# Kernel optimization log

Measured on AMD Instinct MI355X. Metric: run time of the kernel, lower is better.

## Reference

```python
import jax, jax.numpy as jnp
import numpy as np

B, T, F, H = 128, 1024, 256, 512  # batch, seq_len (input_dims[0]), features (input_dims[1]), rnn_size


def _lstm(xWb, U, reverse=False, return_sequences=False):
    """Keras-semantics LSTM. xWb: [B,T,4H] = x @ W + b precomputed. Gate order i,f,g,o."""
    Hn = U.shape[0]
    xs = jnp.swapaxes(xWb, 0, 1)  # [T,B,4H] for scan over time
    h0 = jnp.zeros((xWb.shape[0], Hn), xWb.dtype)
    c0 = h0

    def step(carry, xw):
        h, c = carry
        z = xw + h @ U  # [B,4H]
        i, f, g, o = jnp.split(z, 4, axis=-1)
        i = jax.nn.sigmoid(i)
        f = jax.nn.sigmoid(f)
        g = jnp.tanh(g)
        o = jax.nn.sigmoid(o)
        c = f * c + i * g
        h = o * jnp.tanh(c)
        return (h, c), h

    (hT, _), hs = jax.lax.scan(step, (h0, c0), xs, reverse=reverse)
    if return_sequences:
        return jnp.swapaxes(hs, 0, 1)  # [B,T,H]
    return hT  # [B,H] final state (for reverse=True this is the state after t=0)


def setup_inputs() -> dict:
    key = jax.random.key(0)
    ks = jax.random.split(key, 9)
    g = lambda k, shape: (jax.random.normal(k, shape, jnp.float32) * 0.05)
    return {
        "x": jax.random.uniform(ks[0], (B, T, F), jnp.float32),
        # encoder forward-direction LSTM
        "Wf": g(ks[1], (F, 4 * H)), "Uf": g(ks[2], (H, 4 * H)), "bf": jnp.zeros((4 * H,), jnp.float32),
        # encoder backward-direction LSTM
        "Wb": g(ks[3], (F, 4 * H)), "Ub": g(ks[4], (H, 4 * H)), "bb": jnp.zeros((4 * H,), jnp.float32),
        # decoder LSTM (input is concat latent, 2H wide)
        "Wd": g(ks[5], (2 * H, 4 * H)), "Ud": g(ks[6], (H, 4 * H)), "bd": jnp.zeros((4 * H,), jnp.float32),
        # TimeDistributed Dense
        "Wo": g(ks[7], (H, F)), "bo": jnp.zeros((F,), jnp.float32),
    }


def reference(x, Wf, Uf, bf, Wb, Ub, bb, Wd, Ud, bd, Wo, bo):
    # Encoder: Bidirectional(LSTM(H)) -> concat final states [B, 2H]
    h_fwd = _lstm(x @ Wf + bf, Uf, reverse=False)
    h_bwd = _lstm(x @ Wb + bb, Ub, reverse=True)
    latent = jnp.concatenate([h_fwd, h_bwd], axis=-1)  # [B, 2H]
    # Decoder: RepeatVector(T) -> LSTM(H, return_sequences) -> TimeDistributed(Dense(F))
    rep = jnp.broadcast_to(latent[:, None, :], (x.shape[0], x.shape[1], 2 * H))  # [B,T,2H]
    dec = _lstm(rep @ Wd + bd, Ud, return_sequences=True)  # [B,T,H]
    return dec @ Wo + bo  # [B,T,F]
```

## Files before the change

### kernel.cpp

```cpp
#include <hip/hip_runtime.h>
#include <stdint.h>

typedef unsigned short u16;
typedef short bf16x8 __attribute__((ext_vector_type(8)));
typedef float f32x4  __attribute__((ext_vector_type(4)));
typedef unsigned short u16x8 __attribute__((ext_vector_type(8)));
typedef unsigned int   u32x4 __attribute__((ext_vector_type(4)));

__device__ __forceinline__ u16 f2bf(float f) {
  uint32_t u = __float_as_uint(f);
  return (u16)((u + 0x7FFFu + ((u >> 16) & 1u)) >> 16);
}
__device__ __forceinline__ float fsig(float x) {
  x = fminf(fmaxf(x, -30.f), 30.f);
  return __builtin_amdgcn_rcpf(1.f + __builtin_amdgcn_exp2f(-1.44269504088896f * x));
}
__device__ __forceinline__ float ftanhf(float x) {
  x = fminf(fmaxf(x, -10.f), 10.f);
  float e = __builtin_amdgcn_exp2f(2.88539008177793f * x);
  return (e - 1.f) * __builtin_amdgcn_rcpf(e + 1.f);
}

__device__ __forceinline__ int flag_load(const int* p) {
  int v;
  asm volatile("global_load_dword %0, %1, off sc0 sc1\n\ts_waitcnt vmcnt(0)"
               : "=v"(v) : "v"(p) : "memory");
  return v;
}
__device__ __forceinline__ void flag_store(int* p, int v) {
  asm volatile("global_store_dword %0, %1, off sc0 sc1" :: "v"(p), "v"(v) : "memory");
}
__device__ __forceinline__ uint4 ld_coh_x4(const u16* p) {
  uint4 v;
  asm volatile("global_load_dwordx4 %0, %1, off sc0 sc1" : "=v"(v) : "v"(p) : "memory");
  return v;
}
__device__ __forceinline__ void st_coh_x4(u16* p, u32x4 v) {
  asm volatile("global_store_dwordx4 %0, %1, off sc0 sc1" :: "v"(p), "v"(v) : "memory");
}
__device__ __forceinline__ uint4 ld_x4(const float* p) {
  uint4 v;
  asm volatile("global_load_dwordx4 %0, %1, off" : "=v"(v) : "v"(p) : "memory");
  return v;
}
__device__ __forceinline__ void wait_vm0() {
  asm volatile("s_waitcnt vmcnt(0)" ::: "memory");
}
__device__ __forceinline__ bf16x8 pin_frag(const u16* p) {
  uint4 v;
  asm volatile("global_load_dwordx4 %0, %1, off" : "=v"(v) : "v"(p));
  return __builtin_bit_cast(bf16x8, v);
}
__device__ __forceinline__ void poll_flag(const int* fp, int target) {
  int spins = 0;
  while (flag_load(fp) < target) {
    __builtin_amdgcn_s_sleep(1);
    if (++spins > 200000) break;
  }
}

__global__ void prep_kernel(const float* __restrict__ Wf, const float* __restrict__ Uf, const float* __restrict__ bf,
                            const float* __restrict__ Wb, const float* __restrict__ Ub, const float* __restrict__ bb,
                            const float* __restrict__ Wd, const float* __restrict__ Ud, const float* __restrict__ bd,
                            const float* __restrict__ Wo,
                            u16* __restrict__ encF, u16* __restrict__ encB,
                            u16* __restrict__ udF, u16* __restrict__ wdF, u16* __restrict__ woF,
                            float* __restrict__ biasF, float* __restrict__ biasB, float* __restrict__ biasD,
                            int* __restrict__ flagsAll)
{
  constexpr int NC_ENC = 128 * 24 * 64;
  constexpr int NC_UD  = 128 * 16 * 64;
  constexpr int NC_WD  = 128 * 32 * 64;
  constexpr int NC_WO  = 16 * 16 * 64;
  constexpr int B1 = 2 * NC_ENC;
  constexpr int B2 = B1 + NC_UD;
  constexpr int B3 = B2 + NC_WD;
  constexpr int B4 = B3 + NC_WO;
  constexpr int B5 = B4 + 768;
  constexpr int TOTAL = B5 + 64;

  for (int idx = blockIdx.x * 256 + threadIdx.x; idx < TOTAL; idx += gridDim.x * 256) {
    if (idx < B1) {
      int d = idx / NC_ENC;
      int r = idx - d * NC_ENC;
      int ntg = r / 1536;
      int rem = r - ntg * 1536;
      int kt = rem >> 6, lane = rem & 63;
      int np = ntg * 16 + (lane & 15);
      int col = (np & 3) * 512 + (np >> 2);
      int kb = kt * 32 + (lane >> 4) * 8;
      const float* W = d ? Wb : Wf;
      const float* U = d ? Ub : Uf;
      u16* dst = (d ? encB : encF) + (size_t)r * 8;
      if (kb < 256) {
        const float* s = W + (size_t)kb * 2048 + col;
#pragma unroll
        for (int e = 0; e < 8; ++e) dst[e] = f2bf(s[(size_t)e * 2048]);
      } else {
        const float* s = U + (size_t)(kb - 256) * 2048 + col;
#pragma unroll
        for (int e = 0; e < 8; ++e) dst[e] = f2bf(s[(size_t)e * 2048]);
      }
    } else if (idx < B2) {
      int r = idx - B1;
      int ntg = r / 1024;
      int rem = r - ntg * 1024;
      int kt = rem >> 6, lane = rem & 63;
      int np = ntg * 16 + (lane & 15);
      int col = (np & 3) * 512 + (np >> 2);
      int kb = kt * 32 + (lane >> 4) * 8;
      const float* s = Ud + (size_t)kb * 2048 + col;
      u16* dst = udF + (size_t)r * 8;
#pragma unroll
      for (int e = 0; e < 8; ++e) dst[e] = f2bf(s[(size_t)e * 2048]);
    } else if (idx < B3) {
      int r = idx - B2;
      int ntg = r / 2048;
      int rem = r - ntg * 2048;
      int kt = rem >> 6, lane = rem & 63;
      int np = ntg * 16 + (lane & 15);
      int col = (np & 3) * 512 + (np >> 2);
      int kb = kt * 32 + (lane >> 4) * 8;
      const float* s = Wd + (size_t)kb * 2048 + col;
      u16* dst = wdF + (size_t)r * 8;
#pragma unroll
      for (int e = 0; e < 8; ++e) dst[e] = f2bf(s[(size_t)e * 2048]);
    } else if (idx < B4) {
      int r = idx - B3;
      int nt = r / 1024;
      int rem = r - nt * 1024;
      int kt = rem >> 6, lane = rem & 63;
      int col = nt * 16 + (lane & 15);
      int kb = kt * 32 + (lane >> 4) * 8;
      const float* s = Wo + (size_t)kb * 256 + col;
      u16* dst = woF + (size_t)r * 8;
#pragma unroll
      for (int e = 0; e < 8; ++e) dst[e] = f2bf(s[(size_t)e * 256]);
    } else if (idx < B5) {
      int r = idx - B4;
      int which = r >> 8;
      int j0 = (r & 255) * 8;
      const float* src = (which == 0) ? bf : (which == 1) ? bb : bd;
      float* dstb = (which == 0) ? biasF : (which == 1) ? biasB : biasD;
#pragma unroll
      for (int e = 0; e < 8; ++e) {
        int np = j0 + e;
        dstb[np] = src[(np & 3) * 512 + (np >> 2)];
      }
    } else {
      int r = idx - B5;
#pragma unroll
      for (int e = 0; e < 8; ++e) flagsAll[r * 8 + e] = 0;
    }
  }
}


__global__ __launch_bounds__(256, 1) void enc_kernel(
    const float* __restrict__ x,
    const u16* __restrict__ encF, const u16* __restrict__ encB,
    const float* __restrict__ biasF, const float* __restrict__ biasB,
    float* __restrict__ latent, u16* __restrict__ hbuf, int* __restrict__ flags)
{
  const int bid = blockIdx.x;
  const int g   = bid & 15;
  const int wgi = bid >> 4;
  const int dir = g >> 3;
  const int rowBase = (g & 7) * 16;
  const int tid = threadIdx.x;
  const int lane = tid & 63;
  const int wave = tid >> 6;
  const int l15 = lane & 15;
  const int lk  = lane >> 4;

  __shared__ __attribute__((aligned(16))) u16   xlds[2][16][264];
  __shared__ __attribute__((aligned(16))) u16   Alds[16][520];
  __shared__ __attribute__((aligned(16))) float zlds[4][2][16][20];
  __shared__ __attribute__((aligned(16))) u16   hlds[4][16][8];

  const u16* wsrc = dir ? encB : encF;
  bf16x8 Breg[2][24];
#pragma unroll
  for (int n = 0; n < 2; ++n) {
    const int ntg = wgi * 8 + wave * 2 + n;
    const u16* fb = wsrc + (size_t)(ntg * 1536 + lane) * 8;
#pragma unroll
    for (int kt = 0; kt < 24; ++kt)
      Breg[n][kt] = pin_frag(fb + kt * 512);
  }
  wait_vm0();
  __builtin_amdgcn_sched_barrier(0);

  const float* bias = dir ? biasB : biasF;
  float bias_r[2];
  bias_r[0] = bias[(wgi * 8 + wave * 2 + 0) * 16 + l15];
  bias_r[1] = bias[(wgi * 8 + wave * 2 + 1) * 16 + l15];

  u16* myH = hbuf + (size_t)g * 16384;
  int* myFlags = flags + g * 16;
  const int xr = tid >> 4, xc = tid & 15;
  const int cb = tid >> 2;
  const int cr0 = (tid & 3) * 4;

  {
    const int t0 = dir ? 1023 : 0;
    const float* xp = x + ((size_t)(rowBase + xr) * 1024 + t0) * 256 + xc * 16;
    float4 f0 = *(const float4*)xp;
    float4 f1 = *(const float4*)(xp + 4);
    float4 f2 = *(const float4*)(xp + 8);
    float4 f3 = *(const float4*)(xp + 12);
    u16x8 a, b;
    a[0]=f2bf(f0.x); a[1]=f2bf(f0.y); a[2]=f2bf(f0.z); a[3]=f2bf(f0.w);
    a[4]=f2bf(f1.x); a[5]=f2bf(f1.y); a[6]=f2bf(f1.z); a[7]=f2bf(f1.w);
    b[0]=f2bf(f2.x); b[1]=f2bf(f2.y); b[2]=f2bf(f2.z); b[3]=f2bf(f2.w);
    b[4]=f2bf(f3.x); b[5]=f2bf(f3.y); b[6]=f2bf(f3.z); b[7]=f2bf(f3.w);
    *(u16x8*)&xlds[0][xr][xc * 16] = a;
    *(u16x8*)&xlds[0][xr][xc * 16 + 8] = b;
  }
  __syncthreads();

  float cc0 = 0.f, cc1 = 0.f;

  for (int s = 0; s < 1024; ++s) {
    f32x4 acc0 = {bias_r[0], bias_r[0], bias_r[0], bias_r[0]};
    f32x4 acc1 = {bias_r[1], bias_r[1], bias_r[1], bias_r[1]};
#pragma unroll
    for (int kt = 0; kt < 8; ++kt) {
      bf16x8 av = *(const bf16x8*)&xlds[s & 1][l15][kt * 32 + lk * 8];
      acc0 = __builtin_amdgcn_mfma_f32_16x16x32_bf16(av, Breg[0][kt], acc0, 0, 0, 0);
      acc1 = __builtin_amdgcn_mfma_f32_16x16x32_bf16(av, Breg[1][kt], acc1, 0, 0, 0);
    }

    const int sn = (s + 1 < 1024) ? s + 1 : 1023;
    const int tn = dir ? (1023 - sn) : sn;
    const float* xp = x + ((size_t)(rowBase + xr) * 1024 + tn) * 256 + xc * 16;
    uint4 xq0 = ld_x4(xp);
    uint4 xq1 = ld_x4(xp + 4);
    uint4 xq2 = ld_x4(xp + 8);
    uint4 xq3 = ld_x4(xp + 12);

    if (s > 0) {
      if (tid < 16) poll_flag(&myFlags[tid], s);
      __syncthreads();
      const u16* hs = myH + ((s - 1) & 1) * 8192 + cb * 128 + cr0 * 8;
      uint4 h0 = ld_coh_x4(hs);
      uint4 h1 = ld_coh_x4(hs + 8);
      uint4 h2 = ld_coh_x4(hs + 16);
      uint4 h3 = ld_coh_x4(hs + 24);
      wait_vm0();
      __builtin_amdgcn_sched_barrier(0);
      *(uint4*)&Alds[cr0][cb * 8]     = h0;
      *(uint4*)&Alds[cr0 + 1][cb * 8] = h1;
      *(uint4*)&Alds[cr0 + 2][cb * 8] = h2;
      *(uint4*)&Alds[cr0 + 3][cb * 8] = h3;
      __syncthreads();
#pragma unroll
      for (int kt = 0; kt < 16; ++kt) {
        bf16x8 av = *(const bf16x8*)&Alds[l15][kt * 32 + lk * 8];
        acc0 = __builtin_amdgcn_mfma_f32_16x16x32_bf16(av, Breg[0][kt + 8], acc0, 0, 0, 0);
        acc1 = __builtin_amdgcn_mfma_f32_16x16x32_bf16(av, Breg[1][kt + 8], acc1, 0, 0, 0);
      }
    } else {
      wait_vm0();
      __builtin_amdgcn_sched_barrier(0);
    }

#pragma unroll
    for (int r = 0; r < 4; ++r) {
      zlds[wave][0][lk * 4 + r][l15] = acc0[r];
      zlds[wave][1][lk * 4 + r][l15] = acc1[r];
    }
    asm volatile("s_waitcnt lgkmcnt(0)" ::: "memory");
    float4 g0 = *(const float4*)&zlds[wave][0][l15][lk * 4];
    float4 g1 = *(const float4*)&zlds[wave][1][l15][lk * 4];
    float hv0, hv1;
    { float iv = fsig(g0.x), fv = fsig(g0.y), gg = ftanhf(g0.z), ov = fsig(g0.w);
      cc0 = fv * cc0 + iv * gg;  hv0 = ov * ftanhf(cc0); }
    { float iv = fsig(g1.x), fv = fsig(g1.y), gg = ftanhf(g1.z), ov = fsig(g1.w);
      cc1 = fv * cc1 + iv * gg;  hv1 = ov * ftanhf(cc1); }

    {
      float4 f0 = __builtin_bit_cast(float4, xq0);
      float4 f1 = __builtin_bit_cast(float4, xq1);
      float4 f2 = __builtin_bit_cast(float4, xq2);
      float4 f3 = __builtin_bit_cast(float4, xq3);
      u16x8 a, b;
      a[0]=f2bf(f0.x); a[1]=f2bf(f0.y); a[2]=f2bf(f0.z); a[3]=f2bf(f0.w);
      a[4]=f2bf(f1.x); a[5]=f2bf(f1.y); a[6]=f2bf(f1.z); a[7]=f2bf(f1.w);
      b[0]=f2bf(f2.x); b[1]=f2bf(f2.y); b[2]=f2bf(f2.z); b[3]=f2bf(f2.w);
      b[4]=f2bf(f3.x); b[5]=f2bf(f3.y); b[6]=f2bf(f3.z); b[7]=f2bf(f3.w);
      *(u16x8*)&xlds[(s + 1) & 1][xr][xc * 16] = a;
      *(u16x8*)&xlds[(s + 1) & 1][xr][xc * 16 + 8] = b;
    }

    if (s < 1023) {
      hlds[wave][l15][lk]     = f2bf(hv0);
      hlds[wave][l15][lk + 4] = f2bf(hv1);
      asm volatile("s_waitcnt lgkmcnt(0)" ::: "memory");
      if (lane < 16) {
        const u32x4 c = *(const u32x4*)&hlds[wave][lane][0];
        u16* hw = myH + (s & 1) * 8192 + (wgi * 4 + wave) * 128 + lane * 8;
        st_coh_x4(hw, c);
      }
    } else {
      float* lp = latent + (size_t)(rowBase + l15) * 1024 + dir * 512 + wgi * 32 + wave * 8 + lk;
      lp[0] = hv0;
      lp[4] = hv1;
    }

    wait_vm0();
    __syncthreads();
    if (tid == 0 && s < 1023) flag_store(&myFlags[wgi], s + 1);
  }
}

__global__ __launch_bounds__(256, 1) void dec_kernel(
    const float* __restrict__ latent,
    const u16* __restrict__ udF, const u16* __restrict__ wdF, const u16* __restrict__ woF,
    const float* __restrict__ biasD, const float* __restrict__ bo,
    float* __restrict__ out, u16* __restrict__ hbuf, int* __restrict__ flags)
{
  const int bid = blockIdx.x;
  const int g   = bid & 7;
  const int wgi = bid >> 3;
  const int rowBase = g * 16;
  const int tid = threadIdx.x;
  const int lane = tid & 63;
  const int wave = tid >> 6;
  const int l15 = lane & 15;
  const int lk  = lane >> 4;

  __shared__ __attribute__((aligned(16))) u16   Llds[16][1032];
  __shared__ __attribute__((aligned(16))) u16   Alds[2][16][520];
  __shared__ __attribute__((aligned(16))) float zlds[4][2][16][20];
  __shared__ __attribute__((aligned(16))) u16   hlds[4][16][8];

#pragma unroll
  for (int c8 = 0; c8 < 8; ++c8) {
    const int idx = tid + c8 * 256;
    const int rr = idx >> 7, cf = idx & 127;
    const float* lp = latent + (size_t)(rowBase + rr) * 1024 + cf * 8;
    float4 v0 = *(const float4*)lp;
    float4 v1 = *(const float4*)(lp + 4);
    u16x8 tv;
    tv[0]=f2bf(v0.x); tv[1]=f2bf(v0.y); tv[2]=f2bf(v0.z); tv[3]=f2bf(v0.w);
    tv[4]=f2bf(v1.x); tv[5]=f2bf(v1.y); tv[6]=f2bf(v1.z); tv[7]=f2bf(v1.w);
    *(u16x8*)&Llds[rr][cf * 8] = tv;
  }
  __syncthreads();

  f32x4 xwd[2];
#pragma unroll
  for (int n = 0; n < 2; ++n) {
    const int ntg = wgi * 8 + wave * 2 + n;
    const float br = biasD[ntg * 16 + l15];
    f32x4 xw = {br, br, br, br};
    const u16* wf = wdF + (size_t)(ntg * 2048 + lane) * 8;
#pragma unroll
    for (int kt = 0; kt < 32; ++kt) {
      bf16x8 b = *(const bf16x8*)(wf + kt * 512);
      bf16x8 a = *(const bf16x8*)&Llds[l15][kt * 32 + lk * 8];
      xw = __builtin_amdgcn_mfma_f32_16x16x32_bf16(a, b, xw, 0, 0, 0);
    }
    xwd[n] = xw;
  }

  bf16x8 Bu[2][16];
#pragma unroll
  for (int n = 0; n < 2; ++n) {
    const int ntg = wgi * 8 + wave * 2 + n;
    const u16* ub = udF + (size_t)(ntg * 1024 + lane) * 8;
#pragma unroll
    for (int kt = 0; kt < 16; ++kt)
      Bu[n][kt] = pin_frag(ub + kt * 512);
  }
  bf16x8 Bo[16];
  if (wave == 0) {
    const u16* ob = woF + (size_t)(wgi * 1024 + lane) * 8;
#pragma unroll
    for (int kt = 0; kt < 16; ++kt)
      Bo[kt] = pin_frag(ob + kt * 512);
  }
  wait_vm0();
  __builtin_amdgcn_sched_barrier(0);
  const float bo_r = bo[wgi * 16 + l15];

  u16* myH = hbuf + (size_t)g * 16384;
  int* myFlags = flags + g * 16;
  const int cb = tid >> 2;
  const int cr0 = (tid & 3) * 4;

  float cc0 = 0.f, cc1 = 0.f;

  for (int t = 0; t < 1024; ++t) {
    f32x4 acc0 = xwd[0], acc1 = xwd[1];

    if (t > 0) {
      if (tid < 16) poll_flag(&myFlags[tid], t);
      __syncthreads();
      const u16* hs = myH + ((t - 1) & 1) * 8192 + cb * 128 + cr0 * 8;
      uint4 h0 = ld_coh_x4(hs);
      uint4 h1 = ld_coh_x4(hs + 8);
      uint4 h2 = ld_coh_x4(hs + 16);
      uint4 h3 = ld_coh_x4(hs + 24);
      wait_vm0();
      __builtin_amdgcn_sched_barrier(0);
      *(uint4*)&Alds[t & 1][cr0][cb * 8]     = h0;
      *(uint4*)&Alds[t & 1][cr0 + 1][cb * 8] = h1;
      *(uint4*)&Alds[t & 1][cr0 + 2][cb * 8] = h2;
      *(uint4*)&Alds[t & 1][cr0 + 3][cb * 8] = h3;
      __syncthreads();
#pragma unroll
      for (int kt = 0; kt < 16; ++kt) {
        bf16x8 av = *(const bf16x8*)&Alds[t & 1][l15][kt * 32 + lk * 8];
        acc0 = __builtin_amdgcn_mfma_f32_16x16x32_bf16(av, Bu[0][kt], acc0, 0, 0, 0);
        acc1 = __builtin_amdgcn_mfma_f32_16x16x32_bf16(av, Bu[1][kt], acc1, 0, 0, 0);
      }
    }

#pragma unroll
    for (int r = 0; r < 4; ++r) {
      zlds[wave][0][lk * 4 + r][l15] = acc0[r];
      zlds[wave][1][lk * 4 + r][l15] = acc1[r];
    }
    asm volatile("s_waitcnt lgkmcnt(0)" ::: "memory");
    float4 g0 = *(const float4*)&zlds[wave][0][l15][lk * 4];
    float4 g1 = *(const float4*)&zlds[wave][1][l15][lk * 4];
    float hv0, hv1;
    { float iv = fsig(g0.x), fv = fsig(g0.y), gg = ftanhf(g0.z), ov = fsig(g0.w);
      cc0 = fv * cc0 + iv * gg;  hv0 = ov * ftanhf(cc0); }
    { float iv = fsig(g1.x), fv = fsig(g1.y), gg = ftanhf(g1.z), ov = fsig(g1.w);
      cc1 = fv * cc1 + iv * gg;  hv1 = ov * ftanhf(cc1); }

    {
      hlds[wave][l15][lk]     = f2bf(hv0);
      hlds[wave][l15][lk + 4] = f2bf(hv1);
      asm volatile("s_waitcnt lgkmcnt(0)" ::: "memory");
      if (lane < 16) {
        const u32x4 c = *(const u32x4*)&hlds[wave][lane][0];
        u16* hw = myH + (t & 1) * 8192 + (wgi * 4 + wave) * 128 + lane * 8;
        st_coh_x4(hw, c);
      }
      wait_vm0();
      __syncthreads();
      if (tid == 0) flag_store(&myFlags[wgi], t + 1);
    }

    if (t > 0 && wave == 0) {
      f32x4 od = {bo_r, bo_r, bo_r, bo_r};
#pragma unroll
      for (int kt = 0; kt < 16; ++kt) {
        bf16x8 a = *(const bf16x8*)&Alds[t & 1][l15][kt * 32 + lk * 8];
        od = __builtin_amdgcn_mfma_f32_16x16x32_bf16(a, Bo[kt], od, 0, 0, 0);
      }
#pragma unroll
      for (int r = 0; r < 4; ++r)
        out[((size_t)(rowBase + lk * 4 + r) * 1024 + (t - 1)) * 256 + wgi * 16 + l15] = od[r];
    }
  }

  if (tid < 16) poll_flag(&myFlags[tid], 1024);
  __syncthreads();
  {
    const u16* hs = myH + 8192 + cb * 128 + cr0 * 8;
    uint4 h0 = ld_coh_x4(hs);
    uint4 h1 = ld_coh_x4(hs + 8);
    uint4 h2 = ld_coh_x4(hs + 16);
    uint4 h3 = ld_coh_x4(hs + 24);
    wait_vm0();
    __builtin_amdgcn_sched_barrier(0);
    *(uint4*)&Alds[0][cr0][cb * 8]     = h0;
    *(uint4*)&Alds[0][cr0 + 1][cb * 8] = h1;
    *(uint4*)&Alds[0][cr0 + 2][cb * 8] = h2;
    *(uint4*)&Alds[0][cr0 + 3][cb * 8] = h3;
    __syncthreads();
    if (wave == 0) {
      f32x4 od = {bo_r, bo_r, bo_r, bo_r};
#pragma unroll
      for (int kt = 0; kt < 16; ++kt) {
        bf16x8 a = *(const bf16x8*)&Alds[0][l15][kt * 32 + lk * 8];
        od = __builtin_amdgcn_mfma_f32_16x16x32_bf16(a, Bo[kt], od, 0, 0, 0);
      }
#pragma unroll
      for (int r = 0; r < 4; ++r)
        out[((size_t)(rowBase + lk * 4 + r) * 1024 + 1023) * 256 + wgi * 16 + l15] = od[r];
    }
  }
}

extern "C" void kernel_launch(void* const* d_in, const int* in_sizes, int n_in,
                              void* d_out, int out_size, void* d_ws, size_t ws_size,
                              hipStream_t stream)
{
  const float* x  = (const float*)d_in[0];
  const float* Wf = (const float*)d_in[1];
  const float* Uf = (const float*)d_in[2];
  const float* bf = (const float*)d_in[3];
  const float* Wb = (const float*)d_in[4];
  const float* Ub = (const float*)d_in[5];
  const float* bb = (const float*)d_in[6];
  const float* Wd = (const float*)d_in[7];
  const float* Ud = (const float*)d_in[8];
  const float* bd = (const float*)d_in[9];
  const float* Wo = (const float*)d_in[10];
  const float* bo = (const float*)d_in[11];

  if (ws_size < 14182400) return;

  char* ws = (char*)d_ws;
  u16*  encF   = (u16*)(ws + 0);
  u16*  encB   = (u16*)(ws + 3145728);
  u16*  udF    = (u16*)(ws + 6291456);
  u16*  wdF    = (u16*)(ws + 8388608);
  u16*  woF    = (u16*)(ws + 12582912);
  float* biasF = (float*)(ws + 12845056);
  float* biasB = (float*)(ws + 12853248);
  float* biasD = (float*)(ws + 12861440);
  float* latent= (float*)(ws + 12869632);
  u16*  hbufE  = (u16*)(ws + 13393920);
  u16*  hbufD  = (u16*)(ws + 13918208);
  int*  flagsE = (int*)(ws + 14180352);
  int*  flagsD = (int*)(ws + 14181376);

  prep_kernel<<<256, 256, 0, stream>>>(Wf, Uf, bf, Wb, Ub, bb, Wd, Ud, bd, Wo,
                                       encF, encB, udF, wdF, woF,
                                       biasF, biasB, biasD, flagsE);
  enc_kernel<<<256, 256, 0, stream>>>(x, encF, encB, biasF, biasB, latent, hbufE, flagsE);
  dec_kernel<<<128, 256, 0, stream>>>(latent, udF, wdF, woF, biasD, bo,
                                      (float*)d_out, hbufD, flagsD);
}
```

Baseline: 5.560 ms.

## Embed step tags in h-state low bits to replace flag polling

The LSTM recurrent kernels now write a 4-bit timestep tag into the least-significant mantissa bits of selected bf16 hidden-state values, so consumers can poll the h data directly instead of first waiting on per-workgroup flags and then issuing a second load. Readers spin on the tagged data, check the tag, and fall back to the flag only occasionally. They then clear the low bit before the MMA. The encoder also moves the h store earlier, ahead of the x conversion, so neighbours see it sooner. This costs some precision in the tagged elements, adds a zeroing pass for the h buffers in prep, and relies on 16-byte coherent stores becoming visible atomically.

```diff
diff --git a/kernel.cpp b/kernel.cpp
--- a/kernel.cpp
+++ b/kernel.cpp
@@ -11,6 +11,10 @@
   uint32_t u = __float_as_uint(f);
   return (u16)((u + 0x7FFFu + ((u >> 16) & 1u)) >> 16);
 }
+__device__ __forceinline__ u16 f2bf6(float f) {
+  uint32_t u = __float_as_uint(f);
+  return (u16)(((u + 0xFFFFu + ((u >> 17) & 1u)) >> 17) << 1);
+}
 __device__ __forceinline__ float fsig(float x) {
   x = fminf(fmaxf(x, -30.f), 30.f);
   return __builtin_amdgcn_rcpf(1.f + __builtin_amdgcn_exp2f(-1.44269504088896f * x));
@@ -24,39 +28,40 @@
 __device__ __forceinline__ int flag_load(const int* p) {
   int v;
   asm volatile("global_load_dword %0, %1, off sc0 sc1\n\ts_waitcnt vmcnt(0)"
-               : "=v"(v) : "v"(p) : "memory");
+               : "=&v"(v) : "v"(p) : "memory");
   return v;
 }
 __device__ __forceinline__ void flag_store(int* p, int v) {
   asm volatile("global_store_dword %0, %1, off sc0 sc1" :: "v"(p), "v"(v) : "memory");
 }
-__device__ __forceinline__ uint4 ld_coh_x4(const u16* p) {
-  uint4 v;
-  asm volatile("global_load_dwordx4 %0, %1, off sc0 sc1" : "=v"(v) : "v"(p) : "memory");
-  return v;
+__device__ __forceinline__ void ld_chunk4(const u16* p, u32x4& a, u32x4& b,
+                                          u32x4& c, u32x4& d) {
+  asm volatile("global_load_dwordx4 %0, %4, off sc0 sc1\n\t"
+               "global_load_dwordx4 %1, %4, off offset:16 sc0 sc1\n\t"
+               "global_load_dwordx4 %2, %4, off offset:32 sc0 sc1\n\t"
+               "global_load_dwordx4 %3, %4, off offset:48 sc0 sc1\n\t"
+               "s_waitcnt vmcnt(0)"
+               : "=&v"(a), "=&v"(b), "=&v"(c), "=&v"(d)
+               : "v"(p) : "memory");
 }
 __device__ __forceinline__ void st_coh_x4(u16* p, u32x4 v) {
   asm volatile("global_store_dwordx4 %0, %1, off sc0 sc1" :: "v"(p), "v"(v) : "memory");
 }
 __device__ __forceinline__ uint4 ld_x4(const float* p) {
   uint4 v;
-  asm volatile("global_load_dwordx4 %0, %1, off" : "=v"(v) : "v"(p) : "memory");
+  asm volatile("global_load_dwordx4 %0, %1, off" : "=&v"(v) : "v"(p) : "memory");
   return v;
 }
 __device__ __forceinline__ void wait_vm0() {
   asm volatile("s_waitcnt vmcnt(0)" ::: "memory");
 }
 __device__ __forceinline__ bf16x8 pin_frag(const u16* p) {
-  uint4 v;
-  asm volatile("global_load_dwordx4 %0, %1, off" : "=v"(v) : "v"(p));
+  u32x4 v;
+  asm volatile("global_load_dwordx4 %0, %1, off" : "=&v"(v) : "v"(p));
   return __builtin_bit_cast(bf16x8, v);
 }
-__device__ __forceinline__ void poll_flag(const int* fp, int target) {
-  int spins = 0;
-  while (flag_load(fp) < target) {
-    __builtin_amdgcn_s_sleep(1);
-    if (++spins > 200000) break;
-  }
+__device__ __forceinline__ uint32_t nib_of(u32x4 d) {
+  return (d[0] & 1u) | ((d[1] & 1u) << 1) | ((d[2] & 1u) << 2) | ((d[3] & 1u) << 3);
 }
 
 __global__ void prep_kernel(const float* __restrict__ Wf, const float* __restrict__ Uf, const float* __restrict__ bf,
@@ -66,7 +71,7 @@
                             u16* __restrict__ encF, u16* __restrict__ encB,
                             u16* __restrict__ udF, u16* __restrict__ wdF, u16* __restrict__ woF,
                             float* __restrict__ biasF, float* __restrict__ biasB, float* __restrict__ biasD,
-                            int* __restrict__ flagsAll)
+                            int* __restrict__ flagsAll, u16* __restrict__ hbE, u16* __restrict__ hbD)
 {
   constexpr int NC_ENC = 128 * 24 * 64;
   constexpr int NC_UD  = 128 * 16 * 64;
@@ -77,7 +82,9 @@
   constexpr int B3 = B2 + NC_WD;
   constexpr int B4 = B3 + NC_WO;
   constexpr int B5 = B4 + 768;
-  constexpr int TOTAL = B5 + 64;
+  constexpr int B6 = B5 + 64;
+  constexpr int B7 = B6 + 32768;
+  constexpr int TOTAL = B7 + 16384;
 
   for (int idx = blockIdx.x * 256 + threadIdx.x; idx < TOTAL; idx += gridDim.x * 256) {
     if (idx < B1) {
@@ -147,10 +154,18 @@
         int np = j0 + e;
         dstb[np] = src[(np & 3) * 512 + (np >> 2)];
       }
+    } else if (idx < B6) {
+      int r = idx - B5;
+#pragma unroll
+      for (int e = 0; e < 8; ++e) flagsAll[r * 8 + e] = 0;
+    } else if (idx < B7) {
+      int r = idx - B6;
+      u16x8 z = {0, 0, 0, 0, 0, 0, 0, 0};
+      *(u16x8*)&hbE[(size_t)r * 8] = z;
     } else {
-      int r = idx - B5;
-#pragma unroll
-      for (int e = 0; e < 8; ++e) flagsAll[r * 8 + e] = 0;
+      int r = idx - B7;
+      u16x8 z = {0, 0, 0, 0, 0, 0, 0, 0};
+      *(u16x8*)&hbD[(size_t)r * 8] = z;
     }
   }
 }
@@ -240,19 +255,27 @@
     uint4 xq3 = ld_x4(xp + 12);
 
     if (s > 0) {
-      if (tid < 16) poll_flag(&myFlags[tid], s);
-      __syncthreads();
+      const uint32_t Texp = 8u | ((uint32_t)s & 7u);
       const u16* hs = myH + ((s - 1) & 1) * 8192 + cb * 128 + cr0 * 8;
-      uint4 h0 = ld_coh_x4(hs);
-      uint4 h1 = ld_coh_x4(hs + 8);
-      uint4 h2 = ld_coh_x4(hs + 16);
-      uint4 h3 = ld_coh_x4(hs + 24);
-      wait_vm0();
-      __builtin_amdgcn_sched_barrier(0);
-      *(uint4*)&Alds[cr0][cb * 8]     = h0;
-      *(uint4*)&Alds[cr0 + 1][cb * 8] = h1;
-      *(uint4*)&Alds[cr0 + 2][cb * 8] = h2;
-      *(uint4*)&Alds[cr0 + 3][cb * 8] = h3;
+      const int* pf = &myFlags[tid >> 4];
+      u32x4 h0, h1, h2, h3;
+      int it = 0;
+      while (true) {
+        ld_chunk4(hs, h0, h1, h2, h3);
+        if (nib_of(h0) == Texp && nib_of(h1) == Texp &&
+            nib_of(h2) == Texp && nib_of(h3) == Texp) break;
+        if ((it & 3) == 3 && flag_load(pf) >= s) {
+          ld_chunk4(hs, h0, h1, h2, h3);
+          break;
+        }
+        __builtin_amdgcn_s_sleep(1);
+        if (++it > 200000) break;
+      }
+      h0 &= ~1u; h1 &= ~1u; h2 &= ~1u; h3 &= ~1u;
+      *(u32x4*)&Alds[cr0][cb * 8]     = h0;
+      *(u32x4*)&Alds[cr0 + 1][cb * 8] = h1;
+      *(u32x4*)&Alds[cr0 + 2][cb * 8] = h2;
+      *(u32x4*)&Alds[cr0 + 3][cb * 8] = h3;
       __syncthreads();
 #pragma unroll
       for (int kt = 0; kt < 16; ++kt) {
@@ -278,6 +301,32 @@
       cc0 = fv * cc0 + iv * gg;  hv0 = ov * ftanhf(cc0); }
     { float iv = fsig(g1.x), fv = fsig(g1.y), gg = ftanhf(g1.z), ov = fsig(g1.w);
       cc1 = fv * cc1 + iv * gg;  hv1 = ov * ftanhf(cc1); }
+
+    if (s < 1023) {
+      const uint32_t T = 8u | ((uint32_t)(s + 1) & 7u);
+      u16 v0, v1;
+      if ((lk & 1) == 0) {
+        uint32_t b0 = (lk == 0) ? (T & 1u) : ((T >> 1) & 1u);
+        uint32_t b1 = (lk == 0) ? ((T >> 2) & 1u) : ((T >> 3) & 1u);
+        v0 = f2bf6(hv0) | (u16)b0;
+        v1 = f2bf6(hv1) | (u16)b1;
+      } else {
+        v0 = f2bf(hv0);
+        v1 = f2bf(hv1);
+      }
+      hlds[wave][l15][lk]     = v0;
+      hlds[wave][l15][lk + 4] = v1;
+      asm volatile("s_waitcnt lgkmcnt(0)" ::: "memory");
+      if (lane < 16) {
+        const u32x4 c = *(const u32x4*)&hlds[wave][lane][0];
+        u16* hw = myH + (s & 1) * 8192 + (wgi * 4 + wave) * 128 + lane * 8;
+        st_coh_x4(hw, c);
+      }
+    } else {
+      float* lp = latent + (size_t)(rowBase + l15) * 1024 + dir * 512 + wgi * 32 + wave * 8 + lk;
+      lp[0] = hv0;
+      lp[4] = hv1;
+    }
 
     {
       float4 f0 = __builtin_bit_cast(float4, xq0);
@@ -291,21 +340,6 @@
       b[4]=f2bf(f3.x); b[5]=f2bf(f3.y); b[6]=f2bf(f3.z); b[7]=f2bf(f3.w);
       *(u16x8*)&xlds[(s + 1) & 1][xr][xc * 16] = a;
       *(u16x8*)&xlds[(s + 1) & 1][xr][xc * 16 + 8] = b;
-    }
-
-    if (s < 1023) {
-      hlds[wave][l15][lk]     = f2bf(hv0);
-      hlds[wave][l15][lk + 4] = f2bf(hv1);
-      asm volatile("s_waitcnt lgkmcnt(0)" ::: "memory");
-      if (lane < 16) {
-        const u32x4 c = *(const u32x4*)&hlds[wave][lane][0];
-        u16* hw = myH + (s & 1) * 8192 + (wgi * 4 + wave) * 128 + lane * 8;
-        st_coh_x4(hw, c);
-      }
-    } else {
-      float* lp = latent + (size_t)(rowBase + l15) * 1024 + dir * 512 + wgi * 32 + wave * 8 + lk;
-      lp[0] = hv0;
-      lp[4] = hv1;
     }
 
     wait_vm0();
@@ -396,19 +430,27 @@
     f32x4 acc0 = xwd[0], acc1 = xwd[1];
 
     if (t > 0) {
-      if (tid < 16) poll_flag(&myFlags[tid], t);
-      __syncthreads();
+      const uint32_t Texp = 8u | ((uint32_t)t & 7u);
       const u16* hs = myH + ((t - 1) & 1) * 8192 + cb * 128 + cr0 * 8;
-      uint4 h0 = ld_coh_x4(hs);
-      uint4 h1 = ld_coh_x4(hs + 8);
-      uint4 h2 = ld_coh_x4(hs + 16);
-      uint4 h3 = ld_coh_x4(hs + 24);
-      wait_vm0();
-      __builtin_amdgcn_sched_barrier(0);
-      *(uint4*)&Alds[t & 1][cr0][cb * 8]     = h0;
-      *(uint4*)&Alds[t & 1][cr0 + 1][cb * 8] = h1;
-      *(uint4*)&Alds[t & 1][cr0 + 2][cb * 8] = h2;
-      *(uint4*)&Alds[t & 1][cr0 + 3][cb * 8] = h3;
+      const int* pf = &myFlags[tid >> 4];
+      u32x4 h0, h1, h2, h3;
+      int it = 0;
+      while (true) {
+        ld_chunk4(hs, h0, h1, h2, h3);
+        if (nib_of(h0) == Texp && nib_of(h1) == Texp &&
+            nib_of(h2) == Texp && nib_of(h3) == Texp) break;
+        if ((it & 3) == 3 && flag_load(pf) >= t) {
+          ld_chunk4(hs, h0, h1, h2, h3);
+          break;
+        }
+        __builtin_amdgcn_s_sleep(1);
+        if (++it > 200000) break;
+      }
+      h0 &= ~1u; h1 &= ~1u; h2 &= ~1u; h3 &= ~1u;
+      *(u32x4*)&Alds[t & 1][cr0][cb * 8]     = h0;
+      *(u32x4*)&Alds[t & 1][cr0 + 1][cb * 8] = h1;
+      *(u32x4*)&Alds[t & 1][cr0 + 2][cb * 8] = h2;
+      *(u32x4*)&Alds[t & 1][cr0 + 3][cb * 8] = h3;
       __syncthreads();
 #pragma unroll
       for (int kt = 0; kt < 16; ++kt) {
@@ -433,8 +475,19 @@
       cc1 = fv * cc1 + iv * gg;  hv1 = ov * ftanhf(cc1); }
 
     {
-      hlds[wave][l15][lk]     = f2bf(hv0);
-      hlds[wave][l15][lk + 4] = f2bf(hv1);
+      const uint32_t T = 8u | ((uint32_t)(t + 1) & 7u);
+      u16 v0, v1;
+      if ((lk & 1) == 0) {
+        uint32_t b0 = (lk == 0) ? (T & 1u) : ((T >> 1) & 1u);
+        uint32_t b1 = (lk == 0) ? ((T >> 2) & 1u) : ((T >> 3) & 1u);
+        v0 = f2bf6(hv0) | (u16)b0;
+        v1 = f2bf6(hv1) | (u16)b1;
+      } else {
+        v0 = f2bf(hv0);
+        v1 = f2bf(hv1);
+      }
+      hlds[wave][l15][lk]     = v0;
+      hlds[wave][l15][lk + 4] = v1;
       asm volatile("s_waitcnt lgkmcnt(0)" ::: "memory");
       if (lane < 16) {
         const u32x4 c = *(const u32x4*)&hlds[wave][lane][0];
@@ -459,20 +512,28 @@
     }
   }
 
-  if (tid < 16) poll_flag(&myFlags[tid], 1024);
-  __syncthreads();
   {
+    const uint32_t Texp = 8u;
     const u16* hs = myH + 8192 + cb * 128 + cr0 * 8;
-    uint4 h0 = ld_coh_x4(hs);
-    uint4 h1 = ld_coh_x4(hs + 8);
-    uint4 h2 = ld_coh_x4(hs + 16);
-    uint4 h3 = ld_coh_x4(hs + 24);
-    wait_vm0();
-    __builtin_amdgcn_sched_barrier(0);
-    *(uint4*)&Alds[0][cr0][cb * 8]     = h0;
-    *(uint4*)&Alds[0][cr0 + 1][cb * 8] = h1;
-    *(uint4*)&Alds[0][cr0 + 2][cb * 8] = h2;
-    *(uint4*)&Alds[0][cr0 + 3][cb * 8] = h3;
+    const int* pf = &myFlags[tid >> 4];
+    u32x4 h0, h1, h2, h3;
+    int it = 0;
+    while (true) {
+      ld_chunk4(hs, h0, h1, h2, h3);
+      if (nib_of(h0) == Texp && nib_of(h1) == Texp &&
+          nib_of(h2) == Texp && nib_of(h3) == Texp) break;
+      if ((it & 3) == 3 && flag_load(pf) >= 1024) {
+        ld_chunk4(hs, h0, h1, h2, h3);
+        break;
+      }
+      __builtin_amdgcn_s_sleep(1);
+      if (++it > 200000) break;
+    }
+    h0 &= ~1u; h1 &= ~1u; h2 &= ~1u; h3 &= ~1u;
+    *(u32x4*)&Alds[0][cr0][cb * 8]     = h0;
+    *(u32x4*)&Alds[0][cr0 + 1][cb * 8] = h1;
+    *(u32x4*)&Alds[0][cr0 + 2][cb * 8] = h2;
+    *(u32x4*)&Alds[0][cr0 + 3][cb * 8] = h3;
     __syncthreads();
     if (wave == 0) {
       f32x4 od = {bo_r, bo_r, bo_r, bo_r};
@@ -524,7 +585,7 @@
 
   prep_kernel<<<256, 256, 0, stream>>>(Wf, Uf, bf, Wb, Ub, bb, Wd, Ud, bd, Wo,
                                        encF, encB, udF, wdF, woF,
-                                       biasF, biasB, biasD, flagsE);
+                                       biasF, biasB, biasD, flagsE, hbufE, hbufD);
   enc_kernel<<<256, 256, 0, stream>>>(x, encF, encB, biasF, biasB, latent, hbufE, flagsE);
   dec_kernel<<<128, 256, 0, stream>>>(latent, udF, wdF, woF, biasD, bo,
                                       (float*)d_out, hbufD, flagsD);
```

New measurement: 4.731 ms. 14.9% less time.
